# Performance work log

Hardware: AMD Instinct MI355X
Metric: run time of the kernel (lower is better)

The kernel has to match this reference:

```python
import jax, jax.numpy as jnp
import numpy as np

B, N, HD = 128, 8192, 256


def setup_inputs() -> dict:
    key = jax.random.key(0)
    ks = jax.random.split(key, 12)
    s = 1.0 / np.sqrt(HD)
    return {
        "encoder_outputs": jax.random.normal(ks[0], (B, N, HD), jnp.float32),
        "hidden": jax.random.normal(ks[1], (B, HD), jnp.float32),
        "cell": jax.random.normal(ks[2], (B, HD), jnp.float32),
        "end_node_embed": jax.random.normal(ks[3], (1, HD), jnp.float32),
        "initial_input": jax.random.normal(ks[4], (B, 3 * HD), jnp.float32),
        # LSTMCell params (PyTorch layout: gates ordered i, f, g, o)
        "W_ih": jax.random.uniform(ks[5], (4 * HD, 3 * HD), jnp.float32, -s, s),
        "b_ih": jax.random.uniform(ks[6], (4 * HD,), jnp.float32, -s, s),
        "W_hh": jax.random.uniform(ks[7], (4 * HD, HD), jnp.float32, -s, s),
        "b_hh": jax.random.uniform(ks[8], (4 * HD,), jnp.float32, -s, s),
        # query_transform Linear params
        "Wq": jax.random.uniform(ks[9], (HD, HD), jnp.float32, -s, s),
        "bq": jax.random.uniform(ks[10], (HD,), jnp.float32, -s, s),
        "max_steps": 10,
    }


def reference(encoder_outputs, hidden, cell, end_node_embed, initial_input,
              W_ih, b_ih, W_hh, b_hh, Wq, bq, max_steps):
    # Prediction mode (teacher_indices=None): feed back top-3 gathered embeddings.
    def step(carry, _):
        h, c, x = carry
        gates = x @ W_ih.T + b_ih + h @ W_hh.T + b_hh        # (B, 4*HD)
        i, f, g, o = jnp.split(gates, 4, axis=-1)
        c_new = jax.nn.sigmoid(f) * c + jax.nn.sigmoid(i) * jnp.tanh(g)
        h_new = jax.nn.sigmoid(o) * jnp.tanh(c_new)
        query = h_new @ Wq.T + bq                            # (B, HD)
        logits = jnp.einsum('bd,bnd->bn', query, encoder_outputs)  # (B, N)
        _, top3 = jax.lax.top_k(logits, 3)                   # (B, 3) int32
        vecs = jnp.take_along_axis(encoder_outputs, top3[..., None], axis=1)  # (B, 3, HD)
        x_next = vecs.reshape(x.shape[0], -1)                # (B, 3*HD)
        return (h_new, c_new, x_next), (logits, top3)
    _, (logits_all, idx_all) = jax.lax.scan(
        step, (hidden, cell, initial_input), None, length=max_steps)
    return logits_all, idx_all  # (max_steps, B, N), (max_steps, B, 3)
```

## Files before the change

### kernel.cpp

```cpp
#include <hip/hip_runtime.h>

typedef unsigned short u16;
typedef unsigned int   u32;

#define B_    128
#define N_    8192
#define HD_   256
#define X_    768
#define T_    10
#define SEGS_ 8
#define SEGROWS_ 1024

__device__ float g_h[B_*HD_];
__device__ float g_c[B_*HD_];
__device__ float g_q[B_*HD_];
__device__ float g_pval[B_*SEGS_*3];
__device__ int   g_pidx[B_*SEGS_*3];
__device__ int   g_isf32;

struct P {
  const void *enc, *h0, *c0, *x0, *Wih, *bih, *Whh, *bhh, *Wq, *bq;
  void* out;
};

#define LDSP(x) ((__attribute__((address_space(3))) void*)(x))
#define GLBP(x) ((const __attribute__((address_space(1))) void*)(x))

__device__ __forceinline__ float bf2f(u16 u){ return __uint_as_float(((u32)u)<<16); }
__device__ __forceinline__ float lo2f(u32 w){ return __uint_as_float(w<<16); }
__device__ __forceinline__ float hi2f(u32 w){ return __uint_as_float(w & 0xffff0000u); }
__device__ __forceinline__ u16 f2bf(float f){
  u32 u = __float_as_uint(f);
  u32 r = u + 0x7fffu + ((u>>16)&1u);
  return (u16)(r>>16);
}

template<bool F32>
__device__ __forceinline__ float ld1(const void* p, size_t i){
  if constexpr (F32) return ((const float*)p)[i];
  else               return bf2f(((const u16*)p)[i]);
}

template<bool F32>
__device__ __forceinline__ void st1(void* p, size_t i, float v){
  if constexpr (F32) ((float*)p)[i] = v;
  else               ((u16*)p)[i]   = f2bf(v);
}

template<bool F32>
__device__ __forceinline__ void ld8(const void* p, size_t i, float* o){
  if constexpr (F32){
    const float4* q = (const float4*)((const float*)p + i);
    float4 a = q[0], b = q[1];
    o[0]=a.x; o[1]=a.y; o[2]=a.z; o[3]=a.w;
    o[4]=b.x; o[5]=b.y; o[6]=b.z; o[7]=b.w;
  } else {
    uint4 u = *(const uint4*)((const u16*)p + i);
    o[0]=lo2f(u.x); o[1]=hi2f(u.x); o[2]=lo2f(u.y); o[3]=hi2f(u.y);
    o[4]=lo2f(u.z); o[5]=hi2f(u.z); o[6]=lo2f(u.w); o[7]=hi2f(u.w);
  }
}

__device__ __forceinline__ void t3ins(float v,int i,
    float&v0,int&i0,float&v1,int&i1,float&v2,int&i2){
  if (v>v0 || (v==v0 && i<i0)) { v2=v1;i2=i1; v1=v0;i1=i0; v0=v;i0=i; }
  else if (v>v1 || (v==v1 && i<i1)) { v2=v1;i2=i1; v1=v;i1=i; }
  else if (v>v2 || (v==v2 && i<i2)) { v2=v;i2=i; }
}

__global__ void k_probe(const void* enc){
  const int lane = threadIdx.x;
  const u16 u = ((const u16*)enc)[lane*2];
  const float a = fabsf(bf2f(u));
  const bool inr = (a >= 0.0009765625f) && (a <= 1024.0f);
  unsigned long long m = __ballot(inr ? 1 : 0);
  if (lane==0) g_isf32 = (__popcll(m) < 32) ? 1 : 0;
}

template<bool F32>
__device__ void lstm_b(const P& p, int t, int b)
{
  const int d = threadIdx.x;
  __shared__ float xs[X_];
  __shared__ float hs[HD_];
  __shared__ float hn[HD_];
  __shared__ int   idx3[3];

  float cd;
  if (t == 0){
    for (int i=d;i<X_;i+=256) xs[i] = ld1<F32>(p.x0, (size_t)b*X_+i);
    hs[d] = ld1<F32>(p.h0, (size_t)b*HD_+d);
    cd    = ld1<F32>(p.c0, (size_t)b*HD_+d);
  } else {
    if (d==0){
      float v0=-3.4e38f,v1=-3.4e38f,v2=-3.4e38f; int i0=-1,i1=-1,i2=-1;
      const float* pv = g_pval + b*SEGS_*3;
      const int*   pi = g_pidx + b*SEGS_*3;
      for (int s=0;s<SEGS_*3;s++) t3ins(pv[s],pi[s],v0,i0,v1,i1,v2,i2);
      idx3[0]=i0; idx3[1]=i1; idx3[2]=i2;
      const size_t ib = (size_t)T_*B_*N_ + (size_t)(t-1)*B_*3 + (size_t)b*3;
      st1<F32>(p.out, ib+0, (float)i0);
      st1<F32>(p.out, ib+1, (float)i1);
      st1<F32>(p.out, ib+2, (float)i2);
    }
    __syncthreads();
    #pragma unroll
    for (int j=0;j<3;j++){
      int jj = idx3[j]; jj = jj<0 ? 0 : (jj>N_-1 ? N_-1 : jj);
      xs[j*HD_+d] = ld1<F32>(p.enc, ((size_t)b*N_ + jj)*HD_ + d);
    }
    hs[d] = g_h[b*HD_+d];
    cd    = g_c[b*HD_+d];
  }
  __syncthreads();

  float g4[4];
  #pragma unroll
  for (int gi=0;gi<4;gi++){
    const int row = gi*HD_ + d;
    float acc = ld1<F32>(p.bih,row) + ld1<F32>(p.bhh,row);
    #pragma unroll 4
    for (int kk=0;kk<X_/8;kk++){
      float w[8]; ld8<F32>(p.Wih, (size_t)row*X_ + kk*8, w);
      #pragma unroll
      for (int j=0;j<8;j++) acc = fmaf(xs[kk*8+j], w[j], acc);
    }
    #pragma unroll 4
    for (int kk=0;kk<HD_/8;kk++){
      float w[8]; ld8<F32>(p.Whh, (size_t)row*HD_ + kk*8, w);
      #pragma unroll
      for (int j=0;j<8;j++) acc = fmaf(hs[kk*8+j], w[j], acc);
    }
    g4[gi]=acc;
  }
  const float sig_i = 1.f/(1.f+expf(-g4[0]));
  const float sig_f = 1.f/(1.f+expf(-g4[1]));
  const float tan_g = tanhf(g4[2]);
  const float sig_o = 1.f/(1.f+expf(-g4[3]));
  const float cn = sig_f*cd + sig_i*tan_g;
  const float hv = sig_o*tanhf(cn);
  g_c[b*HD_+d]=cn; g_h[b*HD_+d]=hv; hn[d]=hv;
  __syncthreads();

  float acc = ld1<F32>(p.bq,d);
  #pragma unroll 4
  for (int kk=0;kk<HD_/8;kk++){
    float w[8]; ld8<F32>(p.Wq, (size_t)d*HD_ + kk*8, w);
    #pragma unroll
    for (int j=0;j<8;j++) acc = fmaf(hn[kk*8+j], w[j], acc);
  }
  g_q[b*HD_+d]=acc;
}

__global__ __launch_bounds__(256) void k_lstm(P p, int t)
{
  if (g_isf32) lstm_b<true >(p, t, blockIdx.x);
  else         lstm_b<false>(p, t, blockIdx.x);
}

template<bool F32>
__device__ void logits_b(const P& p, int t, int b, int seg)
{
  __shared__ uint4 tile[2048];
  __shared__ float qs[HD_];
  const int l = threadIdx.x;

  for (int i=l;i<HD_;i+=64) qs[i] = g_q[b*HD_+i];
  __syncthreads();

  float v0=-3.4e38f,v1=-3.4e38f,v2=-3.4e38f; int i0=-1,i1=-1,i2=-1;

  const size_t segelem = ((size_t)b*N_ + (size_t)seg*SEGROWS_)*HD_;
  const size_t obase   = (size_t)t*B_*N_ + (size_t)b*N_ + (size_t)seg*SEGROWS_;

  if constexpr (!F32){
    const u16* encb = (const u16*)p.enc + segelem;
    for (int tl=0; tl<16; ++tl){
      asm volatile("s_waitcnt lgkmcnt(0)" ::: "memory");
      #pragma unroll
      for (int i=0;i<32;i++){
        const int row = 2*i + (l>>5);
        const int ks  = (l & 31) ^ (row & 7);
        const u16* src = encb + ((size_t)(tl*64 + row))*HD_ + ks*8;
        __builtin_amdgcn_global_load_lds(GLBP(src), LDSP(&tile[i*64]), 16, 0, 0);
      }
      asm volatile("s_waitcnt vmcnt(0)" ::: "memory");
      float acc = 0.f;
      #pragma unroll 8
      for (int k=0;k<32;k++){
        uint4 u = tile[(l<<5) + (k ^ (l & 7))];
        const float* qk = &qs[k*8];
        acc = fmaf(lo2f(u.x), qk[0], acc);
        acc = fmaf(hi2f(u.x), qk[1], acc);
        acc = fmaf(lo2f(u.y), qk[2], acc);
        acc = fmaf(hi2f(u.y), qk[3], acc);
        acc = fmaf(lo2f(u.z), qk[4], acc);
        acc = fmaf(hi2f(u.z), qk[5], acc);
        acc = fmaf(lo2f(u.w), qk[6], acc);
        acc = fmaf(hi2f(u.w), qk[7], acc);
      }
      t3ins(acc, seg*SEGROWS_ + tl*64 + l, v0,i0,v1,i1,v2,i2);
      ((u16*)p.out)[obase + tl*64 + l] = f2bf(acc);
    }
  } else {
    const float* encb = (const float*)p.enc + segelem;
    for (int tl=0; tl<32; ++tl){
      asm volatile("s_waitcnt lgkmcnt(0)" ::: "memory");
      #pragma unroll
      for (int i=0;i<32;i++){
        const int row = i;
        const int ks  = l ^ (row & 7);
        const float* src = encb + ((size_t)(tl*32 + row))*HD_ + ks*4;
        __builtin_amdgcn_global_load_lds(GLBP(src), LDSP(&tile[i*64]), 16, 0, 0);
      }
      asm volatile("s_waitcnt vmcnt(0)" ::: "memory");
      const int r  = l & 31;
      const int kh = (l>>5)*32;
      float acc = 0.f;
      #pragma unroll 8
      for (int k=0;k<32;k++){
        const int kk = kh + k;
        uint4 u = tile[(r<<6) + (kk ^ (r & 7))];
        const float* qk = &qs[kk*4];
        acc = fmaf(__uint_as_float(u.x), qk[0], acc);
        acc = fmaf(__uint_as_float(u.y), qk[1], acc);
        acc = fmaf(__uint_as_float(u.z), qk[2], acc);
        acc = fmaf(__uint_as_float(u.w), qk[3], acc);
      }
      acc += __shfl_xor(acc, 32, 64);
      if (l < 32){
        t3ins(acc, seg*SEGROWS_ + tl*32 + r, v0,i0,v1,i1,v2,i2);
        ((float*)p.out)[obase + tl*32 + r] = acc;
      }
    }
  }

  #pragma unroll
  for (int d=1; d<64; d<<=1){
    float w0=__shfl_xor(v0,d,64), w1=__shfl_xor(v1,d,64), w2=__shfl_xor(v2,d,64);
    int   j0=__shfl_xor(i0,d,64), j1=__shfl_xor(i1,d,64), j2=__shfl_xor(i2,d,64);
    t3ins(w0,j0, v0,i0,v1,i1,v2,i2);
    t3ins(w1,j1, v0,i0,v1,i1,v2,i2);
    t3ins(w2,j2, v0,i0,v1,i1,v2,i2);
  }
  if (l==0){
    float* pv = g_pval + (b*SEGS_+seg)*3;
    int*   pi = g_pidx + (b*SEGS_+seg)*3;
    pv[0]=v0; pv[1]=v1; pv[2]=v2;
    pi[0]=i0; pi[1]=i1; pi[2]=i2;
  }
}

__global__ __launch_bounds__(64) void k_logits(P p, int t)
{
  const int b   = blockIdx.x >> 3;
  const int seg = blockIdx.x & 7;
  if (g_isf32) logits_b<true >(p, t, b, seg);
  else         logits_b<false>(p, t, b, seg);
}

template<bool F32>
__device__ void final_b(const P& p, int b)
{
  if (threadIdx.x==0){
    float v0=-3.4e38f,v1=-3.4e38f,v2=-3.4e38f; int i0=-1,i1=-1,i2=-1;
    const float* pv = g_pval + b*SEGS_*3;
    const int*   pi = g_pidx + b*SEGS_*3;
    for (int s=0;s<SEGS_*3;s++) t3ins(pv[s],pi[s],v0,i0,v1,i1,v2,i2);
    const size_t ib = (size_t)T_*B_*N_ + (size_t)(T_-1)*B_*3 + (size_t)b*3;
    st1<F32>(p.out, ib+0, (float)i0);
    st1<F32>(p.out, ib+1, (float)i1);
    st1<F32>(p.out, ib+2, (float)i2);
  }
}

__global__ void k_final(P p)
{
  if (g_isf32) final_b<true >(p, blockIdx.x);
  else         final_b<false>(p, blockIdx.x);
}

extern "C" void kernel_launch(void* const* d_in, const int* in_sizes, int n_in,
                              void* d_out, int out_size, void* d_ws, size_t ws_size,
                              hipStream_t stream)
{
  (void)in_sizes; (void)n_in; (void)out_size; (void)d_ws; (void)ws_size;
  P p;
  p.enc = d_in[0];
  p.h0  = d_in[1];
  p.c0  = d_in[2];
  p.x0  = d_in[4];
  p.Wih = d_in[5];
  p.bih = d_in[6];
  p.Whh = d_in[7];
  p.bhh = d_in[8];
  p.Wq  = d_in[9];
  p.bq  = d_in[10];
  p.out = d_out;

  k_probe<<<dim3(1),dim3(64),0,stream>>>(p.enc);

  for (int t=0;t<T_;t++){
    k_lstm  <<<dim3(B_),        dim3(256),0,stream>>>(p, t);
    k_logits<<<dim3(B_*SEGS_),  dim3(64), 0,stream>>>(p, t);
  }
  k_final<<<dim3(B_),dim3(64),0,stream>>>(p);
}
```

Before: 4.266 ms.

## Double-buffer encoder tiles in logits kernel and split rows into more segments

The logits kernel now splits each batch row into 32 segments of 256 rows instead of 8 of 1024, giving four times as many blocks. The bf16 path double-buffers async global-to-LDS loads, so the next 32-row tile is fetched while the current one is computed. The f32 path drops LDS staging and reads rows directly with float4 loads. The aim is better latency hiding and more parallelism in the memory-bound pass over the encoder outputs. In exchange, the final top-3 merge has more per-segment partials to combine, and the LDS reads in the bf16 path are no longer XOR-swizzled, which may cause bank conflicts.

```diff
diff --git a/kernel.cpp b/kernel.cpp
--- a/kernel.cpp
+++ b/kernel.cpp
@@ -8,8 +8,8 @@
 #define HD_   256
 #define X_    768
 #define T_    10
-#define SEGS_ 8
-#define SEGROWS_ 1024
+#define SEGS_ 32
+#define SEGROWS_ 256
 
 __device__ float g_h[B_*HD_];
 __device__ float g_c[B_*HD_];
@@ -161,7 +161,6 @@
 template<bool F32>
 __device__ void logits_b(const P& p, int t, int b, int seg)
 {
-  __shared__ uint4 tile[2048];
   __shared__ float qs[HD_];
   const int l = threadIdx.x;
 
@@ -169,69 +168,82 @@
   __syncthreads();
 
   float v0=-3.4e38f,v1=-3.4e38f,v2=-3.4e38f; int i0=-1,i1=-1,i2=-1;
-
-  const size_t segelem = ((size_t)b*N_ + (size_t)seg*SEGROWS_)*HD_;
-  const size_t obase   = (size_t)t*B_*N_ + (size_t)b*N_ + (size_t)seg*SEGROWS_;
+  const int rowglob0 = seg*SEGROWS_;
 
   if constexpr (!F32){
-    const u16* encb = (const u16*)p.enc + segelem;
-    for (int tl=0; tl<16; ++tl){
-      asm volatile("s_waitcnt lgkmcnt(0)" ::: "memory");
+    __shared__ uint4 buf[2][1024];
+    const u16* encb = (const u16*)p.enc + ((size_t)b*N_ + (size_t)seg*SEGROWS_)*HD_;
+    u16* outb = (u16*)p.out + (size_t)t*B_*N_ + (size_t)b*N_ + (size_t)seg*SEGROWS_;
+
+    const int r  = l & 31;
+    const int up = l >> 5;
+    float res[8];
+
+    #define STAGE(T) do{                                                      \
+      const u16* s0 = encb + (size_t)(T)*32*HD_ + l*8;                        \
+      _Pragma("unroll")                                                       \
+      for (int i_=0;i_<16;i_++)                                               \
+        __builtin_amdgcn_global_load_lds(GLBP(s0 + i_*512),                   \
+                                         LDSP(&buf[(T)&1][i_*64]), 16, 0, 0); \
+    }while(0)
+
+    #define COMP(T) do{                                                       \
+      const uint4* rowp = &buf[(T)&1][r*32];                                  \
+      float acc_ = 0.f;                                                       \
+      _Pragma("unroll")                                                       \
+      for (int j_=0;j_<16;j_++){                                              \
+        const int s_ = ((j_ + r) & 15) + up*16;                               \
+        uint4 u_ = rowp[s_];                                                  \
+        const float* qk_ = &qs[s_*8];                                         \
+        acc_ = fmaf(lo2f(u_.x), qk_[0], acc_);                                \
+        acc_ = fmaf(hi2f(u_.x), qk_[1], acc_);                                \
+        acc_ = fmaf(lo2f(u_.y), qk_[2], acc_);                                \
+        acc_ = fmaf(hi2f(u_.y), qk_[3], acc_);                                \
+        acc_ = fmaf(lo2f(u_.z), qk_[4], acc_);                                \
+        acc_ = fmaf(hi2f(u_.z), qk_[5], acc_);                                \
+        acc_ = fmaf(lo2f(u_.w), qk_[6], acc_);                                \
+        acc_ = fmaf(hi2f(u_.w), qk_[7], acc_);                                \
+      }                                                                       \
+      acc_ += __shfl_xor(acc_, 32, 64);                                       \
+      res[T] = acc_;                                                          \
+    }while(0)
+
+    STAGE(0);
+    #pragma unroll
+    for (int T=0;T<7;T++){
+      STAGE(T+1);
+      asm volatile("s_waitcnt vmcnt(16)" ::: "memory");
+      COMP(T);
+    }
+    asm volatile("s_waitcnt vmcnt(0)" ::: "memory");
+    COMP(7);
+    #undef STAGE
+    #undef COMP
+
+    if (l < 32){
       #pragma unroll
-      for (int i=0;i<32;i++){
-        const int row = 2*i + (l>>5);
-        const int ks  = (l & 31) ^ (row & 7);
-        const u16* src = encb + ((size_t)(tl*64 + row))*HD_ + ks*8;
-        __builtin_amdgcn_global_load_lds(GLBP(src), LDSP(&tile[i*64]), 16, 0, 0);
+      for (int T=0;T<8;T++){
+        t3ins(res[T], rowglob0 + T*32 + r, v0,i0,v1,i1,v2,i2);
+        outb[T*32 + r] = f2bf(res[T]);
       }
-      asm volatile("s_waitcnt vmcnt(0)" ::: "memory");
+    }
+  } else {
+    const float* encb = (const float*)p.enc + ((size_t)b*N_ + (size_t)seg*SEGROWS_)*HD_;
+    float* outb = (float*)p.out + (size_t)t*B_*N_ + (size_t)b*N_ + (size_t)seg*SEGROWS_;
+    for (int row=l; row<SEGROWS_; row+=64){
+      const float4* rp = (const float4*)(encb + (size_t)row*HD_);
       float acc = 0.f;
       #pragma unroll 8
-      for (int k=0;k<32;k++){
-        uint4 u = tile[(l<<5) + (k ^ (l & 7))];
-        const float* qk = &qs[k*8];
-        acc = fmaf(lo2f(u.x), qk[0], acc);
-        acc = fmaf(hi2f(u.x), qk[1], acc);
-        acc = fmaf(lo2f(u.y), qk[2], acc);
-        acc = fmaf(hi2f(u.y), qk[3], acc);
-        acc = fmaf(lo2f(u.z), qk[4], acc);
-        acc = fmaf(hi2f(u.z), qk[5], acc);
-        acc = fmaf(lo2f(u.w), qk[6], acc);
-        acc = fmaf(hi2f(u.w), qk[7], acc);
+      for (int k=0;k<64;k++){
+        float4 v = rp[k];
+        const float* qk = &qs[k*4];
+        acc = fmaf(v.x, qk[0], acc);
+        acc = fmaf(v.y, qk[1], acc);
+        acc = fmaf(v.z, qk[2], acc);
+        acc = fmaf(v.w, qk[3], acc);
       }
-      t3ins(acc, seg*SEGROWS_ + tl*64 + l, v0,i0,v1,i1,v2,i2);
-      ((u16*)p.out)[obase + tl*64 + l] = f2bf(acc);
-    }
-  } else {
-    const float* encb = (const float*)p.enc + segelem;
-    for (int tl=0; tl<32; ++tl){
-      asm volatile("s_waitcnt lgkmcnt(0)" ::: "memory");
-      #pragma unroll
-      for (int i=0;i<32;i++){
-        const int row = i;
-        const int ks  = l ^ (row & 7);
-        const float* src = encb + ((size_t)(tl*32 + row))*HD_ + ks*4;
-        __builtin_amdgcn_global_load_lds(GLBP(src), LDSP(&tile[i*64]), 16, 0, 0);
-      }
-      asm volatile("s_waitcnt vmcnt(0)" ::: "memory");
-      const int r  = l & 31;
-      const int kh = (l>>5)*32;
-      float acc = 0.f;
-      #pragma unroll 8
-      for (int k=0;k<32;k++){
-        const int kk = kh + k;
-        uint4 u = tile[(r<<6) + (kk ^ (r & 7))];
-        const float* qk = &qs[kk*4];
-        acc = fmaf(__uint_as_float(u.x), qk[0], acc);
-        acc = fmaf(__uint_as_float(u.y), qk[1], acc);
-        acc = fmaf(__uint_as_float(u.z), qk[2], acc);
-        acc = fmaf(__uint_as_float(u.w), qk[3], acc);
-      }
-      acc += __shfl_xor(acc, 32, 64);
-      if (l < 32){
-        t3ins(acc, seg*SEGROWS_ + tl*32 + r, v0,i0,v1,i1,v2,i2);
-        ((float*)p.out)[obase + tl*32 + r] = acc;
-      }
+      t3ins(acc, rowglob0 + row, v0,i0,v1,i1,v2,i2);
+      outb[row] = acc;
     }
   }
 
@@ -253,8 +265,8 @@
 
 __global__ __launch_bounds__(64) void k_logits(P p, int t)
 {
-  const int b   = blockIdx.x >> 3;
-  const int seg = blockIdx.x & 7;
+  const int b   = blockIdx.x >> 5;
+  const int seg = blockIdx.x & 31;
   if (g_isf32) logits_b<true >(p, t, b, seg);
   else         logits_b<false>(p, t, b, seg);
 }
```

Result: slower. 4.424 ms (+3.7%).
